# Kernel tuning notes

Measured on AMD Instinct MI355X. Metric: run time of the kernel, lower is better.

## Reference

```python
import jax, jax.numpy as jnp
import numpy as np

N = 100000      # nodes
E = 1600000     # edges (before self-loops)
F_IN = 16       # num_node_features
HID = 16        # hid
HEADS = 4       # in_head == out_head
B = 64          # num graphs
G = 16          # num_global_features
NEG_SLOPE = 0.2


def gat_conv(x, src, dst, W, a_src, a_dst, b, concat):
    """PyG-style GATConv. x:[N,F], W:[F,H*C], a_src/a_dst:[H,C], b:[H*C] or [C]."""
    n = x.shape[0]
    H, C = a_src.shape
    h = (x @ W).reshape(n, H, C)                       # [N,H,C]
    alpha_s = (h * a_src).sum(-1)                      # [N,H]
    alpha_d = (h * a_dst).sum(-1)                      # [N,H]
    e = jax.nn.leaky_relu(alpha_s[src] + alpha_d[dst], NEG_SLOPE)  # [E',H]
    # segment softmax over destination nodes (stable; max is grad-free)
    m = jax.lax.stop_gradient(jax.ops.segment_max(e, dst, num_segments=n))
    ex = jnp.exp(e - m[dst])
    denom = jax.ops.segment_sum(ex, dst, num_segments=n)
    alpha = ex / (denom[dst] + 1e-16)                  # [E',H]
    out = jax.ops.segment_sum(h[src] * alpha[:, :, None], dst, num_segments=n)  # [N,H,C]
    out = out.reshape(n, H * C) if concat else out.mean(axis=1)
    return out + b


def setup_inputs() -> dict:
    key = jax.random.key(0)
    ks = jax.random.split(key, 24)
    s = 0.1
    inp = {
        "x": jax.random.normal(ks[0], (N, F_IN), jnp.float32),
        "stats": jax.random.normal(ks[1], (B, G), jnp.float32),
        # conv1: F_IN -> HID, heads=HEADS, concat=True
        "W1": jax.random.normal(ks[2], (F_IN, HEADS * HID), jnp.float32) * s,
        "a1s": jax.random.normal(ks[3], (HEADS, HID), jnp.float32) * s,
        "a1d": jax.random.normal(ks[4], (HEADS, HID), jnp.float32) * s,
        "b1": jnp.zeros((HEADS * HID,), jnp.float32),
        # conv2: HID*HEADS -> HID, heads=HEADS, concat=False
        "W2": jax.random.normal(ks[5], (HEADS * HID, HEADS * HID), jnp.float32) * s,
        "a2s": jax.random.normal(ks[6], (HEADS, HID), jnp.float32) * s,
        "a2d": jax.random.normal(ks[7], (HEADS, HID), jnp.float32) * s,
        "b2": jnp.zeros((HID,), jnp.float32),
        # conv3: HID -> HID, heads=HEADS, concat=False
        "W3": jax.random.normal(ks[8], (HID, HEADS * HID), jnp.float32) * s,
        "a3s": jax.random.normal(ks[9], (HEADS, HID), jnp.float32) * s,
        "a3d": jax.random.normal(ks[10], (HEADS, HID), jnp.float32) * s,
        "b3": jnp.zeros((HID,), jnp.float32),
        # MLP head
        "fw1": jax.random.normal(ks[11], (HID + G, 32), jnp.float32) * s,
        "fb1": jnp.zeros((32,), jnp.float32),
        "fw2": jax.random.normal(ks[12], (32, 16), jnp.float32) * s,
        "fb2": jnp.zeros((16,), jnp.float32),
        "fw3": jax.random.normal(ks[13], (16, 1), jnp.float32) * s,
        "fb3": jnp.zeros((1,), jnp.float32),
        "edge_index": jax.random.randint(ks[14], (2, E), 0, N, jnp.int64),
        "batch": jnp.sort(jax.random.randint(ks[15], (N,), 0, B, jnp.int64)),
    }
    return inp


def reference(x, stats, W1, a1s, a1d, b1, W2, a2s, a2d, b2, W3, a3s, a3d, b3,
              fw1, fb1, fw2, fb2, fw3, fb3, edge_index, batch):
    n = x.shape[0]
    loops = jnp.arange(n, dtype=edge_index.dtype)
    src = jnp.concatenate([edge_index[0], loops])  # add_self_loops=True (PyG default)
    dst = jnp.concatenate([edge_index[1], loops])
    h = jax.nn.elu(gat_conv(x, src, dst, W1, a1s, a1d, b1, True))
    h = jax.nn.elu(gat_conv(h, src, dst, W2, a2s, a2d, b2, False))
    h = gat_conv(h, src, dst, W3, a3s, a3d, b3, False)
    nb = stats.shape[0]
    pooled = jax.ops.segment_sum(h, batch, num_segments=nb)
    counts = jax.ops.segment_sum(jnp.ones((n,), h.dtype), batch, num_segments=nb)
    pooled = pooled / jnp.maximum(counts, 1.0)[:, None]   # global_mean_pool
    z = jnp.concatenate([pooled, stats], axis=1)
    z = jax.nn.relu(z @ fw1 + fb1)
    z = jax.nn.relu(z @ fw2 + fb2)
    return z @ fw3 + fb3
```

## Files before the change

### kernel.cpp

```cpp
#include <hip/hip_runtime.h>
#include <hip/hip_bf16.h>
#include <hip/hip_fp16.h>

#define NNODES 100000
#define NEDGES 1600000
#define NB     64
#define NG     16
#define POOL_SLOTS (NB * NG + NB)

#define BKT_SHIFT 7
#define NPB 128
#define NBKT ((NNODES + NPB - 1) / NPB)
#define BCAP 4096
#define SCAT_BLOCKS 256
#define NL1_BLOCKS 2048

typedef float vf2 __attribute__((ext_vector_type(2)));

__device__ __forceinline__ float leaky02(float v) {
    return v > 0.0f ? v : 0.2f * v;
}
__device__ __forceinline__ float elu1(float v) {
    return v > 0.0f ? v : __expf(v) - 1.0f;
}
__device__ __forceinline__ float dot4(float4 a, float4 b) {
    return a.x * b.x + a.y * b.y + a.z * b.z + a.w * b.w;
}

__device__ __forceinline__ int packQ4(float4 v) {
    int pk = __builtin_amdgcn_cvt_pk_fp8_f32(v.x, v.y, 0, false);
    pk = __builtin_amdgcn_cvt_pk_fp8_f32(v.z, v.w, pk, true);
    return pk;
}
__device__ __forceinline__ unsigned char cvt_fp8(float a) {
    int r = __builtin_amdgcn_cvt_pk_fp8_f32(a, a, 0, false);
    return (unsigned char)(r & 0xFF);
}
__device__ __forceinline__ float4 loadQ4(const unsigned char* p) {
    int u = *(const int*)p;
    vf2 lo = __builtin_amdgcn_cvt_pk_f32_fp8(u, false);
    vf2 hi = __builtin_amdgcn_cvt_pk_f32_fp8(u, true);
    return make_float4(lo.x, lo.y, hi.x, hi.y);
}
__device__ __forceinline__ void storeH4(__half* p, float4 v) {
    __half2 a = __floats2half2_rn(v.x, v.y);
    __half2 b = __floats2half2_rn(v.z, v.w);
    uint2 raw;
    raw.x = *reinterpret_cast<unsigned*>(&a);
    raw.y = *reinterpret_cast<unsigned*>(&b);
    *(uint2*)p = raw;
}

__device__ __forceinline__ void nl1_body(const float* __restrict__ X,
                                         const float* __restrict__ W1,
                                         const float* __restrict__ a1s,
                                         const float* __restrict__ a1d,
                                         unsigned char* __restrict__ Xq,
                                         float* __restrict__ AS,
                                         float* __restrict__ AD, int n,
                                         int quad0, int nquads, int q) {
    float ws[4][4], wd[4][4];
#pragma unroll
    for (int h = 0; h < 4; ++h)
#pragma unroll
        for (int j = 0; j < 4; ++j) {
            float s = 0.f, d = 0.f;
            for (int c = 0; c < 16; ++c) {
                float wv = W1[(4 * q + j) * 64 + h * 16 + c];
                s += wv * a1s[h * 16 + c];
                d += wv * a1d[h * 16 + c];
            }
            ws[h][j] = s; wd[h][j] = d;
        }

    for (int i = quad0; i < n; i += nquads) {
        float4 x4 = *(const float4*)(X + (size_t)i * 16 + 4 * q);
        *(int*)(Xq + (size_t)i * 16 + 4 * q) = packQ4(x4);
        float s[4], d[4];
#pragma unroll
        for (int h = 0; h < 4; ++h) {
            s[h] = x4.x * ws[h][0] + x4.y * ws[h][1] + x4.z * ws[h][2] + x4.w * ws[h][3];
            d[h] = x4.x * wd[h][0] + x4.y * wd[h][1] + x4.z * wd[h][2] + x4.w * wd[h][3];
        }
#pragma unroll
        for (int h = 0; h < 4; ++h) {
            s[h] += __shfl_xor(s[h], 1); s[h] += __shfl_xor(s[h], 2);
            d[h] += __shfl_xor(d[h], 1); d[h] += __shfl_xor(d[h], 2);
        }
        if (q == 0) *(float4*)(AS + (size_t)i * 4) = make_float4(s[0], s[1], s[2], s[3]);
        if (q == 1) *(float4*)(AD + (size_t)i * 4) = make_float4(d[0], d[1], d[2], d[3]);
    }
}

__global__ void scatter_nl1(const int* __restrict__ src,
                            const int* __restrict__ dst,
                            int* __restrict__ bucketCnt,
                            unsigned int* __restrict__ pairs, int ne,
                            const float* __restrict__ X,
                            const float* __restrict__ W1,
                            const float* __restrict__ a1s,
                            const float* __restrict__ a1d,
                            unsigned char* __restrict__ Xq,
                            float* __restrict__ AS,
                            float* __restrict__ AD, int n) {
    __shared__ int hist[NBKT];
    __shared__ int base[NBKT];
    int tid = threadIdx.x;

    if (blockIdx.x >= SCAT_BLOCKS) {
        int q = tid & 3;
        int quad0 = ((blockIdx.x - SCAT_BLOCKS) * 256 + tid) >> 2;
        int nquads = (NL1_BLOCKS * 256) >> 2;
        nl1_body(X, W1, a1s, a1d, Xq, AS, AD, n, quad0, nquads, q);
        return;
    }

    for (int i = tid; i < NBKT; i += 256) hist[i] = 0;
    __syncthreads();

    int chunk = (ne + SCAT_BLOCKS - 1) / SCAT_BLOCKS;
    int beg = blockIdx.x * chunk;
    int end = min(beg + chunk, ne);

    for (int e0 = beg; e0 < end; e0 += 1024) {
        int d[4];
#pragma unroll
        for (int q = 0; q < 4; ++q) {
            int e = e0 + q * 256 + tid;
            d[q] = (e < end) ? dst[e] : -1;
        }
#pragma unroll
        for (int q = 0; q < 4; ++q)
            if (d[q] >= 0) atomicAdd(&hist[d[q] >> BKT_SHIFT], 1);
    }
    __syncthreads();

    for (int i = tid; i < NBKT; i += 256) {
        int h = hist[i];
        base[i] = h ? atomicAdd(&bucketCnt[i], h) : 0;
        hist[i] = 0;
    }
    __syncthreads();

    for (int e0 = beg; e0 < end; e0 += 1024) {
        int d[4], s[4];
#pragma unroll
        for (int q = 0; q < 4; ++q) {
            int e = e0 + q * 256 + tid;
            d[q] = (e < end) ? dst[e] : -1;
            s[q] = (e < end) ? src[e] : 0;
        }
        int r[4], bkt[4];
#pragma unroll
        for (int q = 0; q < 4; ++q) {
            if (d[q] >= 0) {
                bkt[q] = d[q] >> BKT_SHIFT;
                r[q] = base[bkt[q]] + atomicAdd(&hist[bkt[q]], 1);
            }
        }
#pragma unroll
        for (int q = 0; q < 4; ++q) {
            if (d[q] >= 0 && r[q] < BCAP)
                pairs[(size_t)bkt[q] * BCAP + r[q]] =
                    (unsigned)s[q] | ((unsigned)(d[q] & (NPB - 1)) << 20);
        }
    }
}

__global__ void bucket_sort(const unsigned int* __restrict__ pairs,
                            const int* __restrict__ bucketCnt,
                            int* __restrict__ srcs,
                            int* __restrict__ indptr, int n) {
    __shared__ int hist[NPB];
    __shared__ int offl[NPB];
    __shared__ int cur[NPB];
    __shared__ int red[256];
    __shared__ int lsrc[BCAP];
    int bkt = blockIdx.x;
    int t = threadIdx.x;
    int cnt = min(bucketCnt[bkt], BCAP);

    int partial = 0;
    for (int j = t; j < bkt; j += 256) partial += min(bucketCnt[j], BCAP);
    red[t] = partial;
    if (t < NPB) hist[t] = 0;
    __syncthreads();
    for (int s = 128; s > 0; s >>= 1) {
        if (t < s) red[t] += red[t + s];
        __syncthreads();
    }
    int boff = red[0];
    if (bkt == NBKT - 1 && t == 0) indptr[n] = boff + cnt;

    const unsigned int* __restrict__ p = pairs + (size_t)bkt * BCAP;
    unsigned int v[BCAP / 256];
#pragma unroll
    for (int i = 0; i < BCAP / 256; ++i) {
        int e = i * 256 + t;
        v[i] = 0u;
        if (e < cnt) {
            v[i] = p[e];
            atomicAdd(&hist[v[i] >> 20], 1);
        }
    }
    __syncthreads();
    if (t < NPB) offl[t] = hist[t];
    __syncthreads();
    for (int off = 1; off < NPB; off <<= 1) {
        int x = 0;
        if (t < NPB && t >= off) x = offl[t - off];
        __syncthreads();
        if (t < NPB && t >= off) offl[t] += x;
        __syncthreads();
    }
    if (t < NPB) {
        int ex = offl[t] - hist[t];
        cur[t] = ex;
        int node = bkt * NPB + t;
        if (node < n) indptr[node] = boff + ex;
    }
    __syncthreads();
#pragma unroll
    for (int i = 0; i < BCAP / 256; ++i) {
        int e = i * 256 + t;
        if (e < cnt) {
            int r = atomicAdd(&cur[v[i] >> 20], 1);
            lsrc[r] = (int)(v[i] & 0xFFFFFu);
        }
    }
    __syncthreads();
    for (int e = t; e < cnt; e += 256) srcs[boff + e] = lsrc[e];
}

__device__ __forceinline__ float4 gat_agg16(
    const unsigned char* __restrict__ Xq, const float* __restrict__ AS,
    const float* __restrict__ AD,
    const int* __restrict__ indptr, const int* __restrict__ srcs,
    int d, int grp, int sl, int head, int dq, float& denOut) {
    float ad  = AD[(size_t)d * 4 + head];
    float asd = AS[(size_t)d * 4 + head];
    float t0 = asd + ad;
    float wself = __expf(leaky02(t0));
    float den = wself;
    float4 x4s = loadQ4(Xq + (size_t)d * 16 + dq * 4);
    float4 acc = make_float4(wself * x4s.x, wself * x4s.y,
                             wself * x4s.z, wself * x4s.w);

    int beg = indptr[d], end = indptr[d + 1];
    for (int e0 = beg; e0 < end; e0 += 16) {
        int cnt = min(16, end - e0);
        int myS = (sl < cnt) ? srcs[e0 + sl] : 0;
        int j = 0;
        for (; j + 4 <= cnt; j += 4) {
            int s[4]; float a[4]; float4 h4[4];
#pragma unroll
            for (int q = 0; q < 4; ++q)
                s[q] = __shfl(myS, (grp << 4) + j + q);
#pragma unroll
            for (int q = 0; q < 4; ++q)
                a[q] = AS[(size_t)s[q] * 4 + head];
#pragma unroll
            for (int q = 0; q < 4; ++q)
                h4[q] = loadQ4(Xq + (size_t)s[q] * 16 + dq * 4);
#pragma unroll
            for (int q = 0; q < 4; ++q) {
                float t = a[q] + ad;
                float w = __expf(leaky02(t));
                den += w;
                acc.x += w * h4[q].x; acc.y += w * h4[q].y;
                acc.z += w * h4[q].z; acc.w += w * h4[q].w;
            }
        }
        for (; j < cnt; ++j) {
            int s = __shfl(myS, (grp << 4) + j);
            float t = AS[(size_t)s * 4 + head] + ad;
            float w = __expf(leaky02(t));
            float4 h4 = loadQ4(Xq + (size_t)s * 16 + dq * 4);
            den += w;
            acc.x += w * h4.x; acc.y += w * h4.y;
            acc.z += w * h4.z; acc.w += w * h4.w;
        }
    }
    denOut = den;
    return acc;
}

__device__ __forceinline__ float4 gat_agg64(
    const unsigned char* __restrict__ H, const float* __restrict__ AS,
    const float* __restrict__ AD,
    const int* __restrict__ indptr, const int* __restrict__ srcs,
    int d, int grp, int sl, int head, float& denOut) {
    float ad  = AD[(size_t)d * 4 + head];
    float asd = AS[(size_t)d * 4 + head];
    float t0 = asd + ad;
    float wself = __expf(leaky02(t0));
    float den = wself;
    float4 h4s = loadQ4(H + (size_t)d * 64 + sl * 4);
    float4 acc = make_float4(wself * h4s.x, wself * h4s.y,
                             wself * h4s.z, wself * h4s.w);

    int beg = indptr[d], end = indptr[d + 1];
    for (int e0 = beg; e0 < end; e0 += 16) {
        int cnt = min(16, end - e0);
        int myS = (sl < cnt) ? srcs[e0 + sl] : 0;
        int j = 0;
        for (; j + 4 <= cnt; j += 4) {
            int s[4]; float a[4]; float4 h4[4];
#pragma unroll
            for (int q = 0; q < 4; ++q)
                s[q] = __shfl(myS, (grp << 4) + j + q);
#pragma unroll
            for (int q = 0; q < 4; ++q)
                a[q] = AS[(size_t)s[q] * 4 + head];
#pragma unroll
            for (int q = 0; q < 4; ++q)
                h4[q] = loadQ4(H + (size_t)s[q] * 64 + sl * 4);
#pragma unroll
            for (int q = 0; q < 4; ++q) {
                float t = a[q] + ad;
                float w = __expf(leaky02(t));
                den += w;
                acc.x += w * h4[q].x; acc.y += w * h4[q].y;
                acc.z += w * h4[q].z; acc.w += w * h4[q].w;
            }
        }
        for (; j < cnt; ++j) {
            int s = __shfl(myS, (grp << 4) + j);
            float t = AS[(size_t)s * 4 + head] + ad;
            float w = __expf(leaky02(t));
            float4 h4 = loadQ4(H + (size_t)s * 64 + sl * 4);
            den += w;
            acc.x += w * h4.x; acc.y += w * h4.y;
            acc.z += w * h4.z; acc.w += w * h4.w;
        }
    }
    denOut = den;
    return acc;
}

__global__ void gat_pull_l1(const unsigned char* __restrict__ Xq,
                            const float* __restrict__ AS,
                            const float* __restrict__ AD,
                            const int* __restrict__ indptr,
                            const int* __restrict__ srcs,
                            const float* __restrict__ W1,
                            const float* __restrict__ bias,
                            __half* __restrict__ out, int n) {
    __shared__ float wlds[16 * 64];
    for (int i = threadIdx.x; i < 16 * 64; i += 256) wlds[i] = W1[i];
    __syncthreads();

    int lane = threadIdx.x & 63;
    int grp = lane >> 4, sl = lane & 15, head = sl >> 2, dq = sl & 3;
    int wave = (blockIdx.x * blockDim.x + threadIdx.x) >> 6;
    int nwaves = (gridDim.x * blockDim.x) >> 6;
    for (int d0 = wave * 4; d0 < n; d0 += nwaves * 4) {
        int d = d0 + grp;
        if (d < n) {
            float den;
            float4 acc = gat_agg16(Xq, AS, AD, indptr, srcs, d, grp, sl, head, dq, den);
            float inv = 1.0f / (den + 1e-16f);
            float4 v = make_float4(acc.x * inv, acc.y * inv, acc.z * inv, acc.w * inv);
            float xin[16];
#pragma unroll
            for (int q = 0; q < 4; ++q) {
                int srcl = (grp << 4) + head * 4 + q;
                xin[4 * q + 0] = __shfl(v.x, srcl);
                xin[4 * q + 1] = __shfl(v.y, srcl);
                xin[4 * q + 2] = __shfl(v.z, srcl);
                xin[4 * q + 3] = __shfl(v.w, srcl);
            }
            float4 o = make_float4(0.f, 0.f, 0.f, 0.f);
#pragma unroll
            for (int k = 0; k < 16; ++k) {
                float4 wr = *(const float4*)&wlds[k * 64 + 4 * sl];
                o.x += xin[k] * wr.x; o.y += xin[k] * wr.y;
                o.z += xin[k] * wr.z; o.w += xin[k] * wr.w;
            }
            float4 b4 = *(const float4*)(bias + 4 * sl);
            o.x = elu1(o.x + b4.x); o.y = elu1(o.y + b4.y);
            o.z = elu1(o.z + b4.z); o.w = elu1(o.w + b4.w);
            storeH4(out + (size_t)d * 64 + sl * 4, o);
        }
    }
}

template <int FIN>
__global__ void node_linear3h(const unsigned* __restrict__ X,
                              const float* __restrict__ W,
                              const float* __restrict__ a_s,
                              const float* __restrict__ a_d,
                              unsigned char* __restrict__ H,
                              float* __restrict__ AS,
                              float* __restrict__ AD, int n) {
    int lane = threadIdx.x & 63;
    int head = lane >> 4;
    int wave = __builtin_amdgcn_readfirstlane(
        (int)((blockIdx.x * blockDim.x + threadIdx.x) >> 6));
    int nwaves = (gridDim.x * blockDim.x) >> 6;

    float w[FIN];
#pragma unroll
    for (int k = 0; k < FIN; ++k) w[k] = W[k * 64 + lane];
    float asl = a_s[lane], adl = a_d[lane];

    for (int i = wave; i < n; i += nwaves) {
        const unsigned* __restrict__ xr = X + (size_t)i * (FIN / 2);
        float acc = 0.0f;
#pragma unroll
        for (int k = 0; k < FIN / 2; ++k) {
            unsigned u = xr[k];
            __half2 hh = *reinterpret_cast<const __half2*>(&u);
            float2 f = __half22float2(hh);
            acc += f.x * w[2 * k] + f.y * w[2 * k + 1];
        }
        H[(size_t)i * 64 + lane] = cvt_fp8(acc);
        float s1 = acc * asl, s2 = acc * adl;
#pragma unroll
        for (int off = 1; off < 16; off <<= 1) {
            s1 += __shfl_xor(s1, off);
            s2 += __shfl_xor(s2, off);
        }
        if ((lane & 15) == 0) {
            AS[(size_t)i * 4 + head] = s1;
            AD[(size_t)i * 4 + head] = s2;
        }
    }
}

__global__ void gat_pull_l2(const unsigned char* __restrict__ H,
                            const float* __restrict__ AS,
                            float* __restrict__ AD,
                            const int* __restrict__ indptr,
                            const int* __restrict__ srcs,
                            const float* __restrict__ bias,
                            const float* __restrict__ W3,
                            const float* __restrict__ a3s,
                            const float* __restrict__ a3d,
                            unsigned char* __restrict__ Xq3,
                            float* __restrict__ AS3, int n) {
    int lane = threadIdx.x & 63;
    int grp = lane >> 4, sl = lane & 15, head = sl >> 2, dq = sl & 3;
    int wave = (blockIdx.x * blockDim.x + threadIdx.x) >> 6;
    int nwaves = (gridDim.x * blockDim.x) >> 6;

    float4 w3s4 = make_float4(0, 0, 0, 0), w3d4 = make_float4(0, 0, 0, 0);
    for (int c = 0; c < 16; ++c) {
        float as_ = a3s[head * 16 + c], ad_ = a3d[head * 16 + c];
        float w0 = W3[(4 * dq + 0) * 64 + head * 16 + c];
        float w1 = W3[(4 * dq + 1) * 64 + head * 16 + c];
        float w2 = W3[(4 * dq + 2) * 64 + head * 16 + c];
        float w3 = W3[(4 * dq + 3) * 64 + head * 16 + c];
        w3s4.x += w0 * as_; w3s4.y += w1 * as_; w3s4.z += w2 * as_; w3s4.w += w3 * as_;
        w3d4.x += w0 * ad_; w3d4.y += w1 * ad_; w3d4.z += w2 * ad_; w3d4.w += w3 * ad_;
    }
    float4 b4 = *(const float4*)(bias + dq * 4);

    for (int d0 = wave * 4; d0 < n; d0 += nwaves * 4) {
        int d = d0 + grp;
        if (d < n) {
            float den;
            float4 acc = gat_agg64(H, AS, AD, indptr, srcs, d, grp, sl, head, den);
            float inv = 1.0f / (den + 1e-16f);
            float4 v = make_float4(acc.x * inv, acc.y * inv, acc.z * inv, acc.w * inv);
#pragma unroll
            for (int off = 4; off <= 8; off <<= 1) {
                v.x += __shfl_xor(v.x, off);
                v.y += __shfl_xor(v.y, off);
                v.z += __shfl_xor(v.z, off);
                v.w += __shfl_xor(v.w, off);
            }
            v.x = elu1(0.25f * v.x + b4.x);
            v.y = elu1(0.25f * v.y + b4.y);
            v.z = elu1(0.25f * v.z + b4.z);
            v.w = elu1(0.25f * v.w + b4.w);
            if (sl < 4)
                *(int*)(Xq3 + (size_t)d * 16 + 4 * sl) = packQ4(v);
            float s1 = dot4(v, w3s4);
            float s2 = dot4(v, w3d4);
            s1 += __shfl_xor(s1, 1); s1 += __shfl_xor(s1, 2);
            s2 += __shfl_xor(s2, 1); s2 += __shfl_xor(s2, 2);
            if (dq == 0) {
                AS3[(size_t)d * 4 + head] = s1;
                AD[(size_t)d * 4 + head] = s2;
            }
        }
    }
}

__global__ void gat_pull_l3(const unsigned char* __restrict__ Xq,
                            const float* __restrict__ AS,
                            const float* __restrict__ AD,
                            const int* __restrict__ indptr,
                            const int* __restrict__ srcs,
                            const float* __restrict__ W3,
                            const float* __restrict__ bias,
                            const int* __restrict__ batch,
                            float* __restrict__ PC, int n) {
    __shared__ float wlds[16 * 64];
    __shared__ float lp[POOL_SLOTS];
    for (int i = threadIdx.x; i < 16 * 64; i += 256) wlds[i] = W3[i];
    for (int i = threadIdx.x; i < POOL_SLOTS; i += 256) lp[i] = 0.f;
    __syncthreads();

    int lane = threadIdx.x & 63;
    int grp = lane >> 4, sl = lane & 15, head = sl >> 2, dq = sl & 3;
    int wave = (blockIdx.x * blockDim.x + threadIdx.x) >> 6;
    int nwaves = (gridDim.x * blockDim.x) >> 6;
    float4 b4 = *(const float4*)(bias + dq * 4);

    for (int d0 = wave * 4; d0 < n; d0 += nwaves * 4) {
        int d = d0 + grp;
        if (d < n) {
            float den;
            float4 acc = gat_agg16(Xq, AS, AD, indptr, srcs, d, grp, sl, head, dq, den);
            float inv = 1.0f / (den + 1e-16f);
            float4 v = make_float4(acc.x * inv, acc.y * inv, acc.z * inv, acc.w * inv);
            float xin[16];
#pragma unroll
            for (int q = 0; q < 4; ++q) {
                int srcl = (grp << 4) + head * 4 + q;
                xin[4 * q + 0] = __shfl(v.x, srcl);
                xin[4 * q + 1] = __shfl(v.y, srcl);
                xin[4 * q + 2] = __shfl(v.z, srcl);
                xin[4 * q + 3] = __shfl(v.w, srcl);
            }
            float4 o = make_float4(0.f, 0.f, 0.f, 0.f);
#pragma unroll
            for (int k = 0; k < 16; ++k) {
                float4 wr = *(const float4*)&wlds[k * 64 + head * 16 + dq * 4];
                o.x += xin[k] * wr.x; o.y += xin[k] * wr.y;
                o.z += xin[k] * wr.z; o.w += xin[k] * wr.w;
            }
#pragma unroll
            for (int off = 4; off <= 8; off <<= 1) {
                o.x += __shfl_xor(o.x, off);
                o.y += __shfl_xor(o.y, off);
                o.z += __shfl_xor(o.z, off);
                o.w += __shfl_xor(o.w, off);
            }
            o.x = 0.25f * o.x + b4.x; o.y = 0.25f * o.y + b4.y;
            o.z = 0.25f * o.z + b4.z; o.w = 0.25f * o.w + b4.w;
            if (sl < 4) {
                int b = batch[d];
                atomicAdd(&lp[b * 16 + sl * 4 + 0], o.x);
                atomicAdd(&lp[b * 16 + sl * 4 + 1], o.y);
                atomicAdd(&lp[b * 16 + sl * 4 + 2], o.z);
                atomicAdd(&lp[b * 16 + sl * 4 + 3], o.w);
                if (sl == 0) atomicAdd(&lp[NB * NG + b], 1.0f);
            }
        }
    }
    __syncthreads();
    for (int i = threadIdx.x; i < POOL_SLOTS; i += 256) {
        float s = lp[i];
        if (s != 0.f) atomicAdd(&PC[i], s);
    }
}

__global__ void mlp_head(const float* __restrict__ pooled_counts,
                         const float* __restrict__ stats,
                         const float* __restrict__ fw1, const float* __restrict__ fb1,
                         const float* __restrict__ fw2, const float* __restrict__ fb2,
                         const float* __restrict__ fw3, const float* __restrict__ fb3,
                         float* __restrict__ out) {
    int g = threadIdx.x;
    if (g >= NB) return;
    const float* pooled = pooled_counts;
    const float* counts = pooled_counts + NB * NG;
    float z[32];
    float inv = 1.0f / fmaxf(counts[g], 1.0f);
#pragma unroll
    for (int c = 0; c < 16; ++c) z[c] = pooled[g * 16 + c] * inv;
#pragma unroll
    for (int c = 0; c < 16; ++c) z[16 + c] = stats[g * 16 + c];

    float z1[32];
#pragma unroll
    for (int j = 0; j < 32; ++j) {
        float acc = fb1[j];
        for (int k = 0; k < 32; ++k) acc += z[k] * fw1[k * 32 + j];
        z1[j] = fmaxf(acc, 0.0f);
    }
    float z2[16];
#pragma unroll
    for (int j = 0; j < 16; ++j) {
        float acc = fb2[j];
        for (int k = 0; k < 32; ++k) acc += z1[k] * fw2[k * 16 + j];
        z2[j] = fmaxf(acc, 0.0f);
    }
    float acc = fb3[0];
#pragma unroll
    for (int k = 0; k < 16; ++k) acc += z2[k] * fw3[k];
    out[g] = acc;
}

extern "C" void kernel_launch(void* const* d_in, const int* in_sizes, int n_in,
                              void* d_out, int out_size, void* d_ws, size_t ws_size,
                              hipStream_t stream) {
    const float* x    = (const float*)d_in[0];
    const float* stats= (const float*)d_in[1];
    const float* W1   = (const float*)d_in[2];
    const float* a1s  = (const float*)d_in[3];
    const float* a1d  = (const float*)d_in[4];
    const float* b1   = (const float*)d_in[5];
    const float* W2   = (const float*)d_in[6];
    const float* a2s  = (const float*)d_in[7];
    const float* a2d  = (const float*)d_in[8];
    const float* b2   = (const float*)d_in[9];
    const float* W3   = (const float*)d_in[10];
    const float* a3s  = (const float*)d_in[11];
    const float* a3d  = (const float*)d_in[12];
    const float* b3   = (const float*)d_in[13];
    const float* fw1  = (const float*)d_in[14];
    const float* fb1  = (const float*)d_in[15];
    const float* fw2  = (const float*)d_in[16];
    const float* fb2  = (const float*)d_in[17];
    const float* fw3  = (const float*)d_in[18];
    const float* fb3  = (const float*)d_in[19];
    const int* ei     = (const int*)d_in[20];
    const int* batch  = (const int*)d_in[21];

    const int n = NNODES, ne = NEDGES;
    const int* srcI = ei;
    const int* dstI = ei + ne;

    unsigned char* Xq = (unsigned char*)d_ws;
    unsigned char* Hq2 = Xq + (size_t)n * 16;
    float* ASa  = (float*)(Hq2 + (size_t)n * 64);
    float* ASb  = ASa + (size_t)n * 4;
    float* AD   = ASb + (size_t)n * 4;
    float* PC   = AD + (size_t)n * 4;
    int* bucketCnt = (int*)(PC + POOL_SLOTS);
    int* indptr    = bucketCnt + NBKT;
    int* srcs      = indptr + (n + 1);
    size_t off = (size_t)((char*)(srcs + ne) - (char*)d_ws);
    off = (off + 255) & ~(size_t)255;
    unsigned int* pairs = (unsigned int*)((char*)d_ws + off);
    __half* B16 = (__half*)pairs;

    const int TB = 256;
    const int nlBlocks   = 2048;
    const int pullBlocks = (n + 15) / 16;

    hipMemsetAsync(PC, 0, (POOL_SLOTS + NBKT) * sizeof(int), stream);

    scatter_nl1<<<SCAT_BLOCKS + NL1_BLOCKS, TB, 0, stream>>>(
        srcI, dstI, bucketCnt, pairs, ne,
        x, W1, a1s, a1d, Xq, ASa, AD, n);
    bucket_sort<<<NBKT, TB, 0, stream>>>(pairs, bucketCnt, srcs, indptr, n);

    gat_pull_l1<<<pullBlocks, TB, 0, stream>>>(Xq, ASa, AD, indptr, srcs,
                                               W1, b1, B16, n);

    node_linear3h<64><<<nlBlocks, TB, 0, stream>>>((const unsigned*)B16, W2,
                                                   a2s, a2d, Hq2, ASb, AD, n);
    gat_pull_l2<<<pullBlocks, TB, 0, stream>>>(Hq2, ASb, AD, indptr, srcs, b2,
                                               W3, a3s, a3d, Xq, ASa, n);
    gat_pull_l3<<<pullBlocks, TB, 0, stream>>>(Xq, ASa, AD, indptr, srcs,
                                               W3, b3, batch, PC, n);

    mlp_head<<<1, 64, 0, stream>>>(PC, stats, fw1, fb1, fw2, fb2, fw3, fb3,
                                   (float*)d_out);
}
```

Measured before the change: 393.9 us.

## Fuse layer-2 linear projection into layer-1 pull kernel and precompute attention folds

The layer-1 aggregation kernel now applies W1, bias and ELU, then immediately multiplies by W2 held in shared memory. It writes the fp8 layer-2 features and their source/destination attention logits directly. This removes the separate node_linear3h launch and the fp16 intermediate buffer round trip through global memory. A tiny fold_prep kernel precomputes W·a attention vectors for layers 1 and 3 once, instead of each thread recomputing them. The cost is 20KB of shared memory per block and more per-node ALU work in the pull kernel, which may reduce occupancy.

```diff
diff --git a/kernel.cpp b/kernel.cpp
--- a/kernel.cpp
+++ b/kernel.cpp
@@ -32,56 +32,47 @@
     pk = __builtin_amdgcn_cvt_pk_fp8_f32(v.z, v.w, pk, true);
     return pk;
 }
-__device__ __forceinline__ unsigned char cvt_fp8(float a) {
-    int r = __builtin_amdgcn_cvt_pk_fp8_f32(a, a, 0, false);
-    return (unsigned char)(r & 0xFF);
-}
 __device__ __forceinline__ float4 loadQ4(const unsigned char* p) {
     int u = *(const int*)p;
     vf2 lo = __builtin_amdgcn_cvt_pk_f32_fp8(u, false);
     vf2 hi = __builtin_amdgcn_cvt_pk_f32_fp8(u, true);
     return make_float4(lo.x, lo.y, hi.x, hi.y);
 }
-__device__ __forceinline__ void storeH4(__half* p, float4 v) {
-    __half2 a = __floats2half2_rn(v.x, v.y);
-    __half2 b = __floats2half2_rn(v.z, v.w);
-    uint2 raw;
-    raw.x = *reinterpret_cast<unsigned*>(&a);
-    raw.y = *reinterpret_cast<unsigned*>(&b);
-    *(uint2*)p = raw;
+
+__global__ void fold_prep(const float* __restrict__ W1,
+                          const float* __restrict__ a1s,
+                          const float* __restrict__ a1d,
+                          const float* __restrict__ W3,
+                          const float* __restrict__ a3s,
+                          const float* __restrict__ a3d,
+                          float* __restrict__ FOLD) {
+    int t = threadIdx.x;
+    int blk = t >> 6, h = (t >> 4) & 3, j = t & 15;
+    const float* W = (blk < 2) ? W1 : W3;
+    const float* a = (blk == 0) ? a1s : (blk == 1) ? a1d : (blk == 2) ? a3s : a3d;
+    float s = 0.f;
+    for (int c = 0; c < 16; ++c) s += W[j * 64 + h * 16 + c] * a[h * 16 + c];
+    FOLD[t] = s;
 }
 
 __device__ __forceinline__ void nl1_body(const float* __restrict__ X,
-                                         const float* __restrict__ W1,
-                                         const float* __restrict__ a1s,
-                                         const float* __restrict__ a1d,
+                                         const float* __restrict__ FOLD,
                                          unsigned char* __restrict__ Xq,
                                          float* __restrict__ AS,
                                          float* __restrict__ AD, int n,
                                          int quad0, int nquads, int q) {
-    float ws[4][4], wd[4][4];
-#pragma unroll
-    for (int h = 0; h < 4; ++h)
-#pragma unroll
-        for (int j = 0; j < 4; ++j) {
-            float s = 0.f, d = 0.f;
-            for (int c = 0; c < 16; ++c) {
-                float wv = W1[(4 * q + j) * 64 + h * 16 + c];
-                s += wv * a1s[h * 16 + c];
-                d += wv * a1d[h * 16 + c];
-            }
-            ws[h][j] = s; wd[h][j] = d;
-        }
-
+    float4 ws[4], wd[4];
+#pragma unroll
+    for (int h = 0; h < 4; ++h) {
+        ws[h] = *(const float4*)&FOLD[h * 16 + 4 * q];
+        wd[h] = *(const float4*)&FOLD[64 + h * 16 + 4 * q];
+    }
     for (int i = quad0; i < n; i += nquads) {
         float4 x4 = *(const float4*)(X + (size_t)i * 16 + 4 * q);
         *(int*)(Xq + (size_t)i * 16 + 4 * q) = packQ4(x4);
         float s[4], d[4];
 #pragma unroll
-        for (int h = 0; h < 4; ++h) {
-            s[h] = x4.x * ws[h][0] + x4.y * ws[h][1] + x4.z * ws[h][2] + x4.w * ws[h][3];
-            d[h] = x4.x * wd[h][0] + x4.y * wd[h][1] + x4.z * wd[h][2] + x4.w * wd[h][3];
-        }
+        for (int h = 0; h < 4; ++h) { s[h] = dot4(x4, ws[h]); d[h] = dot4(x4, wd[h]); }
 #pragma unroll
         for (int h = 0; h < 4; ++h) {
             s[h] += __shfl_xor(s[h], 1); s[h] += __shfl_xor(s[h], 2);
@@ -97,9 +88,7 @@
                             int* __restrict__ bucketCnt,
                             unsigned int* __restrict__ pairs, int ne,
                             const float* __restrict__ X,
-                            const float* __restrict__ W1,
-                            const float* __restrict__ a1s,
-                            const float* __restrict__ a1d,
+                            const float* __restrict__ FOLD,
                             unsigned char* __restrict__ Xq,
                             float* __restrict__ AS,
                             float* __restrict__ AD, int n) {
@@ -111,7 +100,7 @@
         int q = tid & 3;
         int quad0 = ((blockIdx.x - SCAT_BLOCKS) * 256 + tid) >> 2;
         int nquads = (NL1_BLOCKS * 256) >> 2;
-        nl1_body(X, W1, a1s, a1d, Xq, AS, AD, n, quad0, nquads, q);
+        nl1_body(X, FOLD, Xq, AS, AD, n, quad0, nquads, q);
         return;
     }
 
@@ -340,90 +329,82 @@
 
 __global__ void gat_pull_l1(const unsigned char* __restrict__ Xq,
                             const float* __restrict__ AS,
-                            const float* __restrict__ AD,
+                            float* __restrict__ AD,
                             const int* __restrict__ indptr,
                             const int* __restrict__ srcs,
                             const float* __restrict__ W1,
-                            const float* __restrict__ bias,
-                            __half* __restrict__ out, int n) {
-    __shared__ float wlds[16 * 64];
-    for (int i = threadIdx.x; i < 16 * 64; i += 256) wlds[i] = W1[i];
+                            const float* __restrict__ b1,
+                            const float* __restrict__ W2,
+                            const float* __restrict__ a2s,
+                            const float* __restrict__ a2d,
+                            unsigned char* __restrict__ Hq2,
+                            float* __restrict__ AS2, int n) {
+    __shared__ float w1s[16 * 64];
+    __shared__ float w2s[64 * 64];
+    for (int i = threadIdx.x; i < 16 * 64; i += 256) w1s[i] = W1[i];
+    for (int i = threadIdx.x; i < 64 * 64; i += 256) w2s[i] = W2[i];
     __syncthreads();
 
     int lane = threadIdx.x & 63;
     int grp = lane >> 4, sl = lane & 15, head = sl >> 2, dq = sl & 3;
     int wave = (blockIdx.x * blockDim.x + threadIdx.x) >> 6;
     int nwaves = (gridDim.x * blockDim.x) >> 6;
+
     for (int d0 = wave * 4; d0 < n; d0 += nwaves * 4) {
         int d = d0 + grp;
-        if (d < n) {
-            float den;
-            float4 acc = gat_agg16(Xq, AS, AD, indptr, srcs, d, grp, sl, head, dq, den);
-            float inv = 1.0f / (den + 1e-16f);
-            float4 v = make_float4(acc.x * inv, acc.y * inv, acc.z * inv, acc.w * inv);
-            float xin[16];
-#pragma unroll
-            for (int q = 0; q < 4; ++q) {
-                int srcl = (grp << 4) + head * 4 + q;
-                xin[4 * q + 0] = __shfl(v.x, srcl);
-                xin[4 * q + 1] = __shfl(v.y, srcl);
-                xin[4 * q + 2] = __shfl(v.z, srcl);
-                xin[4 * q + 3] = __shfl(v.w, srcl);
-            }
-            float4 o = make_float4(0.f, 0.f, 0.f, 0.f);
-#pragma unroll
-            for (int k = 0; k < 16; ++k) {
-                float4 wr = *(const float4*)&wlds[k * 64 + 4 * sl];
-                o.x += xin[k] * wr.x; o.y += xin[k] * wr.y;
-                o.z += xin[k] * wr.z; o.w += xin[k] * wr.w;
-            }
-            float4 b4 = *(const float4*)(bias + 4 * sl);
-            o.x = elu1(o.x + b4.x); o.y = elu1(o.y + b4.y);
-            o.z = elu1(o.z + b4.z); o.w = elu1(o.w + b4.w);
-            storeH4(out + (size_t)d * 64 + sl * 4, o);
-        }
-    }
-}
-
-template <int FIN>
-__global__ void node_linear3h(const unsigned* __restrict__ X,
-                              const float* __restrict__ W,
-                              const float* __restrict__ a_s,
-                              const float* __restrict__ a_d,
-                              unsigned char* __restrict__ H,
-                              float* __restrict__ AS,
-                              float* __restrict__ AD, int n) {
-    int lane = threadIdx.x & 63;
-    int head = lane >> 4;
-    int wave = __builtin_amdgcn_readfirstlane(
-        (int)((blockIdx.x * blockDim.x + threadIdx.x) >> 6));
-    int nwaves = (gridDim.x * blockDim.x) >> 6;
-
-    float w[FIN];
-#pragma unroll
-    for (int k = 0; k < FIN; ++k) w[k] = W[k * 64 + lane];
-    float asl = a_s[lane], adl = a_d[lane];
-
-    for (int i = wave; i < n; i += nwaves) {
-        const unsigned* __restrict__ xr = X + (size_t)i * (FIN / 2);
-        float acc = 0.0f;
-#pragma unroll
-        for (int k = 0; k < FIN / 2; ++k) {
-            unsigned u = xr[k];
-            __half2 hh = *reinterpret_cast<const __half2*>(&u);
-            float2 f = __half22float2(hh);
-            acc += f.x * w[2 * k] + f.y * w[2 * k + 1];
-        }
-        H[(size_t)i * 64 + lane] = cvt_fp8(acc);
-        float s1 = acc * asl, s2 = acc * adl;
-#pragma unroll
-        for (int off = 1; off < 16; off <<= 1) {
-            s1 += __shfl_xor(s1, off);
-            s2 += __shfl_xor(s2, off);
-        }
-        if ((lane & 15) == 0) {
-            AS[(size_t)i * 4 + head] = s1;
-            AD[(size_t)i * 4 + head] = s2;
+        if (d >= n) continue;
+        float den;
+        float4 acc = gat_agg16(Xq, AS, AD, indptr, srcs, d, grp, sl, head, dq, den);
+        float inv = 1.0f / (den + 1e-16f);
+        float4 v = make_float4(acc.x * inv, acc.y * inv, acc.z * inv, acc.w * inv);
+
+        float4 o = make_float4(0.f, 0.f, 0.f, 0.f);
+#pragma unroll
+        for (int p = 0; p < 4; ++p) {
+            int srcl = (grp << 4) + head * 4 + p;
+            float4 xq;
+            xq.x = __shfl(v.x, srcl); xq.y = __shfl(v.y, srcl);
+            xq.z = __shfl(v.z, srcl); xq.w = __shfl(v.w, srcl);
+            const float* wr = &w1s[(4 * p) * 64 + 4 * sl];
+            float4 w0 = *(const float4*)(wr);
+            float4 w1r = *(const float4*)(wr + 64);
+            float4 w2r = *(const float4*)(wr + 128);
+            float4 w3r = *(const float4*)(wr + 192);
+            o.x += xq.x * w0.x + xq.y * w1r.x + xq.z * w2r.x + xq.w * w3r.x;
+            o.y += xq.x * w0.y + xq.y * w1r.y + xq.z * w2r.y + xq.w * w3r.y;
+            o.z += xq.x * w0.z + xq.y * w1r.z + xq.z * w2r.z + xq.w * w3r.z;
+            o.w += xq.x * w0.w + xq.y * w1r.w + xq.z * w2r.w + xq.w * w3r.w;
+        }
+        float4 bb = *(const float4*)(b1 + 4 * sl);
+        o.x = elu1(o.x + bb.x); o.y = elu1(o.y + bb.y);
+        o.z = elu1(o.z + bb.z); o.w = elu1(o.w + bb.w);
+
+        float4 h2 = make_float4(0.f, 0.f, 0.f, 0.f);
+#pragma unroll 4
+        for (int p = 0; p < 16; ++p) {
+            int srcl = (grp << 4) + p;
+            float c0 = __shfl(o.x, srcl), c1v = __shfl(o.y, srcl);
+            float c2v = __shfl(o.z, srcl), c3v = __shfl(o.w, srcl);
+            const float* wr = &w2s[(4 * p) * 64 + 4 * sl];
+            float4 w0 = *(const float4*)(wr);
+            float4 w1r = *(const float4*)(wr + 64);
+            float4 w2r = *(const float4*)(wr + 128);
+            float4 w3r = *(const float4*)(wr + 192);
+            h2.x += c0 * w0.x + c1v * w1r.x + c2v * w2r.x + c3v * w3r.x;
+            h2.y += c0 * w0.y + c1v * w1r.y + c2v * w2r.y + c3v * w3r.y;
+            h2.z += c0 * w0.z + c1v * w1r.z + c2v * w2r.z + c3v * w3r.z;
+            h2.w += c0 * w0.w + c1v * w1r.w + c2v * w2r.w + c3v * w3r.w;
+        }
+        *(int*)(Hq2 + (size_t)d * 64 + 4 * sl) = packQ4(h2);
+
+        float4 as4 = *(const float4*)(a2s + head * 16 + 4 * dq);
+        float4 ad4 = *(const float4*)(a2d + head * 16 + 4 * dq);
+        float s1 = dot4(h2, as4), s2 = dot4(h2, ad4);
+        s1 += __shfl_xor(s1, 1); s1 += __shfl_xor(s1, 2);
+        s2 += __shfl_xor(s2, 1); s2 += __shfl_xor(s2, 2);
+        if (dq == 0) {
+            AS2[(size_t)d * 4 + head] = s1;
+            AD[(size_t)d * 4 + head] = s2;
         }
     }
 }
@@ -434,9 +415,7 @@
                             const int* __restrict__ indptr,
                             const int* __restrict__ srcs,
                             const float* __restrict__ bias,
-                            const float* __restrict__ W3,
-                            const float* __restrict__ a3s,
-                            const float* __restrict__ a3d,
+                            const float* __restrict__ FOLD,
                             unsigned char* __restrict__ Xq3,
                             float* __restrict__ AS3, int n) {
     int lane = threadIdx.x & 63;
@@ -444,46 +423,37 @@
     int wave = (blockIdx.x * blockDim.x + threadIdx.x) >> 6;
     int nwaves = (gridDim.x * blockDim.x) >> 6;
 
-    float4 w3s4 = make_float4(0, 0, 0, 0), w3d4 = make_float4(0, 0, 0, 0);
-    for (int c = 0; c < 16; ++c) {
-        float as_ = a3s[head * 16 + c], ad_ = a3d[head * 16 + c];
-        float w0 = W3[(4 * dq + 0) * 64 + head * 16 + c];
-        float w1 = W3[(4 * dq + 1) * 64 + head * 16 + c];
-        float w2 = W3[(4 * dq + 2) * 64 + head * 16 + c];
-        float w3 = W3[(4 * dq + 3) * 64 + head * 16 + c];
-        w3s4.x += w0 * as_; w3s4.y += w1 * as_; w3s4.z += w2 * as_; w3s4.w += w3 * as_;
-        w3d4.x += w0 * ad_; w3d4.y += w1 * ad_; w3d4.z += w2 * ad_; w3d4.w += w3 * ad_;
-    }
+    float4 w3s4 = *(const float4*)&FOLD[128 + head * 16 + 4 * dq];
+    float4 w3d4 = *(const float4*)&FOLD[192 + head * 16 + 4 * dq];
     float4 b4 = *(const float4*)(bias + dq * 4);
 
     for (int d0 = wave * 4; d0 < n; d0 += nwaves * 4) {
         int d = d0 + grp;
-        if (d < n) {
-            float den;
-            float4 acc = gat_agg64(H, AS, AD, indptr, srcs, d, grp, sl, head, den);
-            float inv = 1.0f / (den + 1e-16f);
-            float4 v = make_float4(acc.x * inv, acc.y * inv, acc.z * inv, acc.w * inv);
-#pragma unroll
-            for (int off = 4; off <= 8; off <<= 1) {
-                v.x += __shfl_xor(v.x, off);
-                v.y += __shfl_xor(v.y, off);
-                v.z += __shfl_xor(v.z, off);
-                v.w += __shfl_xor(v.w, off);
-            }
-            v.x = elu1(0.25f * v.x + b4.x);
-            v.y = elu1(0.25f * v.y + b4.y);
-            v.z = elu1(0.25f * v.z + b4.z);
-            v.w = elu1(0.25f * v.w + b4.w);
-            if (sl < 4)
-                *(int*)(Xq3 + (size_t)d * 16 + 4 * sl) = packQ4(v);
-            float s1 = dot4(v, w3s4);
-            float s2 = dot4(v, w3d4);
-            s1 += __shfl_xor(s1, 1); s1 += __shfl_xor(s1, 2);
-            s2 += __shfl_xor(s2, 1); s2 += __shfl_xor(s2, 2);
-            if (dq == 0) {
-                AS3[(size_t)d * 4 + head] = s1;
-                AD[(size_t)d * 4 + head] = s2;
-            }
+        if (d >= n) continue;
+        float den;
+        float4 acc = gat_agg64(H, AS, AD, indptr, srcs, d, grp, sl, head, den);
+        float inv = 1.0f / (den + 1e-16f);
+        float4 v = make_float4(acc.x * inv, acc.y * inv, acc.z * inv, acc.w * inv);
+#pragma unroll
+        for (int off = 4; off <= 8; off <<= 1) {
+            v.x += __shfl_xor(v.x, off);
+            v.y += __shfl_xor(v.y, off);
+            v.z += __shfl_xor(v.z, off);
+            v.w += __shfl_xor(v.w, off);
+        }
+        v.x = elu1(0.25f * v.x + b4.x);
+        v.y = elu1(0.25f * v.y + b4.y);
+        v.z = elu1(0.25f * v.z + b4.z);
+        v.w = elu1(0.25f * v.w + b4.w);
+        if (sl < 4)
+            *(int*)(Xq3 + (size_t)d * 16 + 4 * sl) = packQ4(v);
+        float s1 = dot4(v, w3s4);
+        float s2 = dot4(v, w3d4);
+        s1 += __shfl_xor(s1, 1); s1 += __shfl_xor(s1, 2);
+        s2 += __shfl_xor(s2, 1); s2 += __shfl_xor(s2, 2);
+        if (dq == 0) {
+            AS3[(size_t)d * 4 + head] = s1;
+            AD[(size_t)d * 4 + head] = s2;
         }
     }
 }
@@ -497,9 +467,9 @@
                             const float* __restrict__ bias,
                             const int* __restrict__ batch,
                             float* __restrict__ PC, int n) {
-    __shared__ float wlds[16 * 64];
+    __shared__ float w3lds[16 * 64];
     __shared__ float lp[POOL_SLOTS];
-    for (int i = threadIdx.x; i < 16 * 64; i += 256) wlds[i] = W3[i];
+    for (int i = threadIdx.x; i < 16 * 64; i += 256) w3lds[i] = W3[i];
     for (int i = threadIdx.x; i < POOL_SLOTS; i += 256) lp[i] = 0.f;
     __syncthreads();
 
@@ -516,21 +486,22 @@
             float4 acc = gat_agg16(Xq, AS, AD, indptr, srcs, d, grp, sl, head, dq, den);
             float inv = 1.0f / (den + 1e-16f);
             float4 v = make_float4(acc.x * inv, acc.y * inv, acc.z * inv, acc.w * inv);
-            float xin[16];
-#pragma unroll
-            for (int q = 0; q < 4; ++q) {
-                int srcl = (grp << 4) + head * 4 + q;
-                xin[4 * q + 0] = __shfl(v.x, srcl);
-                xin[4 * q + 1] = __shfl(v.y, srcl);
-                xin[4 * q + 2] = __shfl(v.z, srcl);
-                xin[4 * q + 3] = __shfl(v.w, srcl);
-            }
             float4 o = make_float4(0.f, 0.f, 0.f, 0.f);
 #pragma unroll
-            for (int k = 0; k < 16; ++k) {
-                float4 wr = *(const float4*)&wlds[k * 64 + head * 16 + dq * 4];
-                o.x += xin[k] * wr.x; o.y += xin[k] * wr.y;
-                o.z += xin[k] * wr.z; o.w += xin[k] * wr.w;
+            for (int p = 0; p < 4; ++p) {
+                int srcl = (grp << 4) + head * 4 + p;
+                float4 xq;
+                xq.x = __shfl(v.x, srcl); xq.y = __shfl(v.y, srcl);
+                xq.z = __shfl(v.z, srcl); xq.w = __shfl(v.w, srcl);
+                const float* wr = &w3lds[(4 * p) * 64 + head * 16 + 4 * dq];
+                float4 w0 = *(const float4*)(wr);
+                float4 w1r = *(const float4*)(wr + 64);
+                float4 w2r = *(const float4*)(wr + 128);
+                float4 w3r = *(const float4*)(wr + 192);
+                o.x += xq.x * w0.x + xq.y * w1r.x + xq.z * w2r.x + xq.w * w3r.x;
+                o.y += xq.x * w0.y + xq.y * w1r.y + xq.z * w2r.y + xq.w * w3r.y;
+                o.z += xq.x * w0.z + xq.y * w1r.z + xq.z * w2r.z + xq.w * w3r.z;
+                o.w += xq.x * w0.w + xq.y * w1r.w + xq.z * w2r.w + xq.w * w3r.w;
             }
 #pragma unroll
             for (int off = 4; off <= 8; off <<= 1) {
@@ -630,33 +601,33 @@
     float* ASa  = (float*)(Hq2 + (size_t)n * 64);
     float* ASb  = ASa + (size_t)n * 4;
     float* AD   = ASb + (size_t)n * 4;
-    float* PC   = AD + (size_t)n * 4;
+    float* FOLD = AD + (size_t)n * 4;
+    float* PC   = FOLD + 256;
     int* bucketCnt = (int*)(PC + POOL_SLOTS);
     int* indptr    = bucketCnt + NBKT;
     int* srcs      = indptr + (n + 1);
     size_t off = (size_t)((char*)(srcs + ne) - (char*)d_ws);
     off = (off + 255) & ~(size_t)255;
     unsigned int* pairs = (unsigned int*)((char*)d_ws + off);
-    __half* B16 = (__half*)pairs;
 
     const int TB = 256;
-    const int nlBlocks   = 2048;
     const int pullBlocks = (n + 15) / 16;
 
     hipMemsetAsync(PC, 0, (POOL_SLOTS + NBKT) * sizeof(int), stream);
 
+    fold_prep<<<1, 256, 0, stream>>>(W1, a1s, a1d, W3, a3s, a3d, FOLD);
+
     scatter_nl1<<<SCAT_BLOCKS + NL1_BLOCKS, TB, 0, stream>>>(
-        srcI, dstI, bucketCnt, pairs, ne,
-        x, W1, a1s, a1d, Xq, ASa, AD, n);
+        srcI, dstI, bucketCnt, pairs, ne, x, FOLD, Xq, ASa, AD, n);
     bucket_sort<<<NBKT, TB, 0, stream>>>(pairs, bucketCnt, srcs, indptr, n);
 
     gat_pull_l1<<<pullBlocks, TB, 0, stream>>>(Xq, ASa, AD, indptr, srcs,
-                                               W1, b1, B16, n);
-
-    node_linear3h<64><<<nlBlocks, TB, 0, stream>>>((const unsigned*)B16, W2,
-                                                   a2s, a2d, Hq2, ASb, AD, n);
+                                               W1, b1, W2, a2s, a2d,
+                                               Hq2, ASb, n);
+
     gat_pull_l2<<<pullBlocks, TB, 0, stream>>>(Hq2, ASb, AD, indptr, srcs, b2,
-                                               W3, a3s, a3d, Xq, ASa, n);
+                                               FOLD, Xq, ASa, n);
+
     gat_pull_l3<<<pullBlocks, TB, 0, stream>>>(Xq, ASa, AD, indptr, srcs,
                                                W3, b3, batch, PC, n);
 
```

After: 318.1 us, median of 2. -19.2%, faster.
